# Kernel optimization log

Hardware: AMD Instinct MI355X
Metric: run time of the kernel (lower is better)

## Reference

```python
import jax, jax.numpy as jnp
import numpy as np

B, S, H, V, NL = 64, 2048, 512, 50257, 2

def setup_inputs() -> dict:
    key = jax.random.key(0)
    ks = jax.random.split(key, 20)
    s = 0.02
    return {
        "input_ids": jax.random.randint(ks[0], (B,), 0, V),
        "hidden": jax.random.normal(ks[1], (NL, B, H), jnp.float32),
        "block_attn_weights": jax.random.uniform(ks[2], (B, 32), jnp.float32),
        "encoder_outputs": jax.random.normal(ks[3], (B, S, H), jnp.float32),
        "n_blocks": 32,
        "emb": jax.random.normal(ks[4], (V, H), jnp.float32) * s,
        "attn_W": jax.random.normal(ks[5], (H, H), jnp.float32) * s,
        "attn_b": jnp.zeros((H,), jnp.float32),
        "W_ih0": jax.random.normal(ks[6], (3 * H, 2 * H), jnp.float32) * s,
        "W_hh0": jax.random.normal(ks[7], (3 * H, H), jnp.float32) * s,
        "b_ih0": jnp.zeros((3 * H,), jnp.float32),
        "b_hh0": jnp.zeros((3 * H,), jnp.float32),
        "W_ih1": jax.random.normal(ks[8], (3 * H, H), jnp.float32) * s,
        "W_hh1": jax.random.normal(ks[9], (3 * H, H), jnp.float32) * s,
        "b_ih1": jnp.zeros((3 * H,), jnp.float32),
        "b_hh1": jnp.zeros((3 * H,), jnp.float32),
        "out_W": jax.random.normal(ks[10], (V, 2 * H), jnp.float32) * s,
        "out_b": jnp.zeros((V,), jnp.float32),
    }

def _gru_cell(x, h, W_ih, W_hh, b_ih, b_hh):
    gx = x @ W_ih.T + b_ih            # [B, 3H]
    gh = h @ W_hh.T + b_hh            # [B, 3H]
    xr, xz, xn = jnp.split(gx, 3, axis=-1)
    hr, hz, hn = jnp.split(gh, 3, axis=-1)
    r = jax.nn.sigmoid(xr + hr)
    z = jax.nn.sigmoid(xz + hz)
    n = jnp.tanh(xn + r * hn)
    return (1.0 - z) * n + z * h

def reference(input_ids, hidden, block_attn_weights, encoder_outputs, n_blocks,
              emb, attn_W, attn_b, W_ih0, W_hh0, b_ih0, b_hh0,
              W_ih1, W_hh1, b_ih1, b_hh1, out_W, out_b):
    b, s, h = encoder_outputs.shape
    L = s // n_blocks
    eo = encoder_outputs.reshape(b, n_blocks, L, h)          # [B,N,L,H]
    # Luong general score: h_dec . (W e + b), per block
    energy = jnp.einsum('bnlh,gh->bnlg', eo, attn_W) + attn_b  # [B,N,L,H]
    scores = jnp.einsum('bh,bnlh->bnl', hidden[-1], energy)    # [B,N,L]
    attn_w = jax.nn.softmax(scores, axis=-1)                   # [B,N,L]
    block_ctx = jnp.einsum('bnl,bnlh->bnh', attn_w, eo)        # [B,N,H]
    context = jnp.einsum('bn,bnh->bh', block_attn_weights, block_ctx)  # [B,H]
    embedded = emb[input_ids]                                  # [B,H]
    x = jnp.concatenate([embedded, context], axis=-1)          # [B,2H]
    h0 = _gru_cell(x, hidden[0], W_ih0, W_hh0, b_ih0, b_hh0)
    h1 = _gru_cell(h0, hidden[1], W_ih1, W_hh1, b_ih1, b_hh1)
    new_hidden = jnp.stack([h0, h1], axis=0)                   # [NL,B,H]
    out_in = jnp.concatenate([h1, context], axis=-1)           # [B,2H]
    log_probs = jax.nn.log_softmax(out_in @ out_W.T + out_b, axis=-1)  # [B,V]
    return (log_probs, new_hidden, context, attn_w)
```

## Files before the change

### kernel.cpp

```cpp
#include <hip/hip_runtime.h>

#define B_  64
#define S_  2048
#define H_  512
#define V_  50257
#define NB_ 32
#define L_  64
#define H3_ 1536

typedef float  f32x4  __attribute__((ext_vector_type(4)));
typedef __bf16 bf16x8 __attribute__((ext_vector_type(8)));

struct alignas(16) U4 { unsigned int x, y, z, w; };

__device__ __forceinline__ unsigned int f2bf_bits(float f) {
  unsigned int u = __float_as_uint(f);
  return (u + 0x7fffu + ((u >> 16) & 1u)) >> 16;
}

__device__ __forceinline__ f32x4 ntload4(const float* p) {
  return __builtin_nontemporal_load((const f32x4*)p);
}

__device__ __forceinline__ float wave_sum(float v) {
#pragma unroll
  for (int off = 32; off > 0; off >>= 1) v += __shfl_xor(v, off, 64);
  return v;
}

__global__ __launch_bounds__(128) void k_q(const float* __restrict__ hidden,
                                           const float* __restrict__ attn_W,
                                           float* __restrict__ q) {
  __shared__ float sh[4 * H_];
  int tid = threadIdx.x;
  int h  = blockIdx.x * 128 + tid;
  int b0 = blockIdx.y * 4;
  const float* h1 = hidden + B_ * H_;
  for (int i = tid; i < 4 * H_; i += 128) sh[i] = h1[b0 * H_ + i];
  __syncthreads();
  float acc[4] = {0.f, 0.f, 0.f, 0.f};
  for (int g = 0; g < H_; ++g) {
    float w = attn_W[(size_t)g * H_ + h];
#pragma unroll
    for (int bb = 0; bb < 4; ++bb) acc[bb] += sh[bb * H_ + g] * w;
  }
#pragma unroll
  for (int bb = 0; bb < 4; ++bb) q[(b0 + bb) * H_ + h] = acc[bb];
}

__global__ __launch_bounds__(256) void k_attn(
    const float* __restrict__ eo, const float* __restrict__ hidden,
    const float* __restrict__ attn_b, const float* __restrict__ q,
    float* __restrict__ bc, float* __restrict__ attnw_out) {
  __shared__ float sm[4], ss[4];
  __shared__ float shA[4][H_];
  int tid = threadIdx.x;
  int wv = tid >> 6, lane = tid & 63;
  int idx = blockIdx.x;
  int b = idx >> 5, n = idx & 31;

  f32x4 q0 = *(const f32x4*)(q + (size_t)b * H_ + lane * 4);
  f32x4 q1 = *(const f32x4*)(q + (size_t)b * H_ + 256 + lane * 4);

  const float* hp = hidden + (size_t)B_ * H_ + (size_t)b * H_;
  f32x4 hx = *(const f32x4*)(hp + lane * 4);
  f32x4 hy = *(const f32x4*)(hp + 256 + lane * 4);
  f32x4 ax = *(const f32x4*)(attn_b + lane * 4);
  f32x4 ay = *(const f32x4*)(attn_b + 256 + lane * 4);
  float c0 = hx.x*ax.x + hx.y*ax.y + hx.z*ax.z + hx.w*ax.w
           + hy.x*ay.x + hy.y*ay.y + hy.z*ay.z + hy.w*ay.w;
  c0 = wave_sum(c0);

  const float* eb = eo + (size_t)(b * NB_ + n) * L_ * H_;
  float m = -1e30f, s = 0.f, myscore = 0.f;
  f32x4 A0 = {0,0,0,0}, A1 = {0,0,0,0};
  for (int lr = 0; lr < 16; lr += 2) {
    const float* rA = eb + (size_t)(wv * 16 + lr) * H_;
    const float* rB = rA + H_;
    f32x4 a0 = ntload4(rA + lane * 4);
    f32x4 a1 = ntload4(rA + 256 + lane * 4);
    f32x4 b0 = ntload4(rB + lane * 4);
    f32x4 b1 = ntload4(rB + 256 + lane * 4);
    float pa = a0.x*q0.x + a0.y*q0.y + a0.z*q0.z + a0.w*q0.w
             + a1.x*q1.x + a1.y*q1.y + a1.z*q1.z + a1.w*q1.w;
    float pb = b0.x*q0.x + b0.y*q0.y + b0.z*q0.z + b0.w*q0.w
             + b1.x*q1.x + b1.y*q1.y + b1.z*q1.z + b1.w*q1.w;
#pragma unroll
    for (int off = 32; off > 0; off >>= 1) {
      pa += __shfl_xor(pa, off, 64);
      pb += __shfl_xor(pb, off, 64);
    }
    pa += c0; pb += c0;
    if (lane == lr)     myscore = pa;
    if (lane == lr + 1) myscore = pb;
    float mnew  = fmaxf(m, fmaxf(pa, pb));
    float alpha = __expf(m - mnew);
    float wa    = __expf(pa - mnew);
    float wb    = __expf(pb - mnew);
    s = s * alpha + wa + wb;
    A0.x = A0.x*alpha + wa*a0.x + wb*b0.x;
    A0.y = A0.y*alpha + wa*a0.y + wb*b0.y;
    A0.z = A0.z*alpha + wa*a0.z + wb*b0.z;
    A0.w = A0.w*alpha + wa*a0.w + wb*b0.w;
    A1.x = A1.x*alpha + wa*a1.x + wb*b1.x;
    A1.y = A1.y*alpha + wa*a1.y + wb*b1.y;
    A1.z = A1.z*alpha + wa*a1.z + wb*b1.z;
    A1.w = A1.w*alpha + wa*a1.w + wb*b1.w;
    m = mnew;
  }
  if (lane == 0) { sm[wv] = m; ss[wv] = s; }
  __syncthreads();
  float m_g = fmaxf(fmaxf(sm[0], sm[1]), fmaxf(sm[2], sm[3]));
  float s_g = ss[0]*__expf(sm[0]-m_g) + ss[1]*__expf(sm[1]-m_g)
            + ss[2]*__expf(sm[2]-m_g) + ss[3]*__expf(sm[3]-m_g);
  float scale = __expf(m - m_g);
  f32x4* pa4 = (f32x4*)&shA[wv][0];
  f32x4 w0 = {A0.x*scale, A0.y*scale, A0.z*scale, A0.w*scale};
  f32x4 w1 = {A1.x*scale, A1.y*scale, A1.z*scale, A1.w*scale};
  pa4[lane] = w0; pa4[64 + lane] = w1;
  __syncthreads();
  float inv = 1.f / s_g;
  float2 sum = {0.f, 0.f};
#pragma unroll
  for (int w = 0; w < 4; ++w) {
    float2 v = ((float2*)&shA[w][0])[tid];
    sum.x += v.x; sum.y += v.y;
  }
  float2* bv = (float2*)(bc + (size_t)(b * NB_ + n) * H_);
  bv[tid] = (float2){sum.x * inv, sum.y * inv};
  if (lane < 16)
    attnw_out[(size_t)(b * NB_ + n) * L_ + wv * 16 + lane] =
        __expf(myscore - m_g) * inv;
}

__global__ __launch_bounds__(512) void k_prep(
    const int* __restrict__ ids, const float* __restrict__ hidden,
    const float* __restrict__ baw, const float* __restrict__ emb,
    const float* __restrict__ bc, float* __restrict__ ctx,
    unsigned short* __restrict__ xcatb, unsigned short* __restrict__ h0b,
    unsigned short* __restrict__ h1b, float* __restrict__ out_ctx) {
  int b = blockIdx.x, h = threadIdx.x;
  int id = ids[b];
  float ev = emb[(size_t)id * H_ + h];
  float acc = 0.f;
  for (int n = 0; n < NB_; ++n)
    acc += baw[b * NB_ + n] * bc[(size_t)(b * NB_ + n) * H_ + h];
  ctx[b * H_ + h]      = acc;
  out_ctx[b * H_ + h]  = acc;
  xcatb[b * 1024 + h]        = (unsigned short)f2bf_bits(ev);
  xcatb[b * 1024 + 512 + h]  = (unsigned short)f2bf_bits(acc);
  h0b[b * H_ + h] = (unsigned short)f2bf_bits(hidden[b * H_ + h]);
  h1b[b * H_ + h] = (unsigned short)f2bf_bits(hidden[B_ * H_ + b * H_ + h]);
}

__global__ __launch_bounds__(256) void k_mv2(
    const float* __restrict__ W1, const float* __restrict__ bias1,
    const unsigned short* __restrict__ A1, float* __restrict__ C1, int K1,
    const float* __restrict__ W2, const float* __restrict__ bias2,
    const unsigned short* __restrict__ A2, float* __restrict__ C2, int K2) {
  bool sec = blockIdx.x >= 96;
  const float* W = sec ? W2 : W1;
  const float* bias = sec ? bias2 : bias1;
  const unsigned short* A = sec ? A2 : A1;
  float* C = sec ? C2 : C1;
  int K = sec ? K2 : K1;
  int blk = sec ? blockIdx.x - 96 : blockIdx.x;

  int tid = threadIdx.x;
  int wv = tid >> 6, lane = tid & 63;
  int mrow = lane & 15, qd = lane >> 4;
  int j = blk * 16 + mrow;
  const unsigned short* ap = A + (size_t)(wv * 16 + mrow) * K + qd * 8;
  const float* wp = W + (size_t)j * K + qd * 8;
  f32x4 acc = (f32x4){0.f, 0.f, 0.f, 0.f};
  for (int k0 = 0; k0 < K; k0 += 32) {
    bf16x8 af = __builtin_bit_cast(bf16x8, *(const U4*)(ap + k0));
    f32x4 w0 = *(const f32x4*)(wp + k0);
    f32x4 w1 = *(const f32x4*)(wp + k0 + 4);
    U4 braw;
    braw.x = f2bf_bits(w0.x) | (f2bf_bits(w0.y) << 16);
    braw.y = f2bf_bits(w0.z) | (f2bf_bits(w0.w) << 16);
    braw.z = f2bf_bits(w1.x) | (f2bf_bits(w1.y) << 16);
    braw.w = f2bf_bits(w1.z) | (f2bf_bits(w1.w) << 16);
    bf16x8 bf = __builtin_bit_cast(bf16x8, braw);
    acc = __builtin_amdgcn_mfma_f32_16x16x32_bf16(af, bf, acc, 0, 0, 0);
  }
  float bv = bias[j];
#pragma unroll
  for (int r = 0; r < 4; ++r) {
    int brow = wv * 16 + qd * 4 + r;
    C[(size_t)brow * H3_ + j] = acc[r] + bv;
  }
}

__global__ __launch_bounds__(256) void k_out(
    const float* __restrict__ W, const float* __restrict__ bias,
    const unsigned short* __restrict__ A, float* __restrict__ C) {
  int tid = threadIdx.x;
  int wv = tid >> 6, lane = tid & 63;
  int mrow = lane & 15, qd = lane >> 4;
  int j = blockIdx.x * 64 + wv * 16 + mrow;
  int jc = j < V_ ? j : V_ - 1;
  const float* wp = W + (size_t)jc * 1024 + qd * 8;
  const unsigned short* ap = A + mrow * 1024 + qd * 8;
  f32x4 acc[4];
#pragma unroll
  for (int r = 0; r < 4; ++r) acc[r] = (f32x4){0.f, 0.f, 0.f, 0.f};
  for (int k0 = 0; k0 < 1024; k0 += 32) {
    f32x4 w0 = ntload4(wp + k0);
    f32x4 w1 = ntload4(wp + k0 + 4);
    U4 braw;
    braw.x = f2bf_bits(w0.x) | (f2bf_bits(w0.y) << 16);
    braw.y = f2bf_bits(w0.z) | (f2bf_bits(w0.w) << 16);
    braw.z = f2bf_bits(w1.x) | (f2bf_bits(w1.y) << 16);
    braw.w = f2bf_bits(w1.z) | (f2bf_bits(w1.w) << 16);
    bf16x8 bw = __builtin_bit_cast(bf16x8, braw);
#pragma unroll
    for (int r = 0; r < 4; ++r) {
      bf16x8 af = __builtin_bit_cast(bf16x8, *(const U4*)(ap + r * 16 * 1024 + k0));
      acc[r] = __builtin_amdgcn_mfma_f32_16x16x32_bf16(af, bw, acc[r], 0, 0, 0);
    }
  }
  if (j < V_) {
    float bv = bias[j];
#pragma unroll
    for (int r = 0; r < 4; ++r) {
#pragma unroll
      for (int g = 0; g < 4; ++g) {
        int brow = r * 16 + qd * 4 + g;
        C[(size_t)brow * V_ + j] = acc[r][g] + bv;
      }
    }
  }
}

__global__ __launch_bounds__(512) void k_gru(
    const float* __restrict__ gx, const float* __restrict__ gh,
    const float* __restrict__ hprev, float* __restrict__ hnew_out,
    unsigned short* __restrict__ hnew_bf, const float* __restrict__ ctx,
    unsigned short* __restrict__ outin) {
  int b = blockIdx.x, i = threadIdx.x;
  size_t g0 = (size_t)b * H3_ + i;
  float xr = gx[g0], xz = gx[g0 + 512], xn = gx[g0 + 1024];
  float hr = gh[g0], hz = gh[g0 + 512], hn = gh[g0 + 1024];
  float r  = 1.f / (1.f + __expf(-(xr + hr)));
  float z  = 1.f / (1.f + __expf(-(xz + hz)));
  float nn = tanhf(xn + r * hn);
  float hp = hprev[b * H_ + i];
  float h  = (1.f - z) * nn + z * hp;
  hnew_out[b * H_ + i] = h;
  hnew_bf[b * H_ + i]  = (unsigned short)f2bf_bits(h);
  if (outin) {
    outin[b * 1024 + i]       = (unsigned short)f2bf_bits(h);
    outin[b * 1024 + 512 + i] = (unsigned short)f2bf_bits(ctx[b * H_ + i]);
  }
}

__global__ __launch_bounds__(1024) void k_lsm(const float* __restrict__ logits,
                                              float* __restrict__ out) {
  int b = blockIdx.x, tid = threadIdx.x;
  int lane = tid & 63, wid = tid >> 6;
  const float* row = logits + (size_t)b * V_;
  __shared__ float redm[16], reds[16], bl[1];
  float m_t = -1e30f, s_t = 0.f;
  for (int j = tid; j < V_; j += 1024) {
    float x = row[j];
    if (x > m_t) {
      s_t = s_t * __expf(m_t - x) + 1.f;
      m_t = x;
    } else {
      s_t += __expf(x - m_t);
    }
  }
#pragma unroll
  for (int off = 32; off > 0; off >>= 1) {
    float mo = __shfl_xor(m_t, off, 64);
    float so = __shfl_xor(s_t, off, 64);
    float mn = fmaxf(m_t, mo);
    s_t = s_t * __expf(m_t - mn) + so * __expf(mo - mn);
    m_t = mn;
  }
  if (lane == 0) { redm[wid] = m_t; reds[wid] = s_t; }
  __syncthreads();
  if (tid == 0) {
    float m_g = redm[0], s_g = reds[0];
    for (int i = 1; i < 16; ++i) {
      float mn = fmaxf(m_g, redm[i]);
      s_g = s_g * __expf(m_g - mn) + reds[i] * __expf(redm[i] - mn);
      m_g = mn;
    }
    bl[0] = m_g + logf(s_g);
  }
  __syncthreads();
  float lse = bl[0];
  float* orow = out + (size_t)b * V_;
  for (int j = tid; j < V_; j += 1024)
    __builtin_nontemporal_store(row[j] - lse, orow + j);
}

extern "C" void kernel_launch(void* const* d_in, const int* in_sizes, int n_in,
                              void* d_out, int out_size, void* d_ws, size_t ws_size,
                              hipStream_t stream) {
  const int*   ids    = (const int*)d_in[0];
  const float* hidden = (const float*)d_in[1];
  const float* baw    = (const float*)d_in[2];
  const float* eo     = (const float*)d_in[3];
  const float* emb    = (const float*)d_in[5];
  const float* attn_W = (const float*)d_in[6];
  const float* attn_b = (const float*)d_in[7];
  const float* W_ih0  = (const float*)d_in[8];
  const float* W_hh0  = (const float*)d_in[9];
  const float* b_ih0  = (const float*)d_in[10];
  const float* b_hh0  = (const float*)d_in[11];
  const float* W_ih1  = (const float*)d_in[12];
  const float* W_hh1  = (const float*)d_in[13];
  const float* b_ih1  = (const float*)d_in[14];
  const float* b_hh1  = (const float*)d_in[15];
  const float* out_W  = (const float*)d_in[16];
  const float* out_b  = (const float*)d_in[17];
  float* out = (float*)d_out;

  char* ws = (char*)d_ws;
  float*          q      = (float*)(ws + 0);
  float*          bc     = (float*)(ws + 131072);
  float*          ctx    = (float*)(ws + 4325376);
  unsigned short* xcatb  = (unsigned short*)(ws + 4456448);
  unsigned short* h0b    = (unsigned short*)(ws + 4587520);
  unsigned short* h1b    = (unsigned short*)(ws + 4653056);
  unsigned short* h0nb   = (unsigned short*)(ws + 4718592);
  unsigned short* outinb = (unsigned short*)(ws + 4784128);
  float*          gx     = (float*)(ws + 4915200);
  float*          gh     = (float*)(ws + 5308416);
  float*          logits = (float*)(ws + 5701632);

  float* out_lp   = out;
  float* out_nh   = out + 3216448;
  float* out_ctx  = out + 3281984;
  float* out_attw = out + 3314752;

  k_q   <<<dim3(4, 16), 128, 0, stream>>>(hidden, attn_W, q);
  k_attn<<<2048, 256, 0, stream>>>(eo, hidden, attn_b, q, bc, out_attw);
  k_prep<<<64, 512, 0, stream>>>(ids, hidden, baw, emb, bc, ctx, xcatb, h0b, h1b, out_ctx);

  k_mv2<<<192, 256, 0, stream>>>(W_ih0, b_ih0, xcatb, gx, 1024,
                                 W_hh0, b_hh0, h0b,   gh, 512);
  k_gru<<<64, 512, 0, stream>>>(gx, gh, hidden, out_nh, h0nb,
                                (const float*)nullptr, (unsigned short*)nullptr);

  k_mv2<<<192, 256, 0, stream>>>(W_ih1, b_ih1, h0nb, gx, 512,
                                 W_hh1, b_hh1, h1b,  gh, 512);
  k_gru<<<64, 512, 0, stream>>>(gx, gh, hidden + B_ * H_, out_nh + B_ * H_, h0nb,
                                ctx, outinb);

  k_out<<<786, 256, 0, stream>>>(out_W, out_b, outinb, logits);
  k_lsm<<<64, 1024, 0, stream>>>(logits, out_lp);
}
```

Before: 690.7 us.

## Fuse per-block softmax stats into output GEMM and widen attention blocks

The output projection kernel now computes per-block row max and sum-exp partials and writes them to workspace. A small kernel combines these into a per-row log-sum-exp, and a wide elementwise kernel then writes logits minus lse. This replaces the 64-block log-softmax that read the logits twice with low parallelism. Separately, the attention kernel moves to 512 threads with 8 waves, each handling 8 rows instead of 16, to raise parallelism per block. The cost is an extra launch plus a shared-memory reduction and syncthreads at the end of the output GEMM.

```diff
diff --git a/kernel.cpp b/kernel.cpp
--- a/kernel.cpp
+++ b/kernel.cpp
@@ -7,6 +7,7 @@
 #define NB_ 32
 #define L_  64
 #define H3_ 1536
+#define NBLK_OUT 786
 
 typedef float  f32x4  __attribute__((ext_vector_type(4)));
 typedef __bf16 bf16x8 __attribute__((ext_vector_type(8)));
@@ -48,12 +49,12 @@
   for (int bb = 0; bb < 4; ++bb) q[(b0 + bb) * H_ + h] = acc[bb];
 }
 
-__global__ __launch_bounds__(256) void k_attn(
+__global__ __launch_bounds__(512) void k_attn(
     const float* __restrict__ eo, const float* __restrict__ hidden,
     const float* __restrict__ attn_b, const float* __restrict__ q,
     float* __restrict__ bc, float* __restrict__ attnw_out) {
-  __shared__ float sm[4], ss[4];
-  __shared__ float shA[4][H_];
+  __shared__ float sm[8], ss[8];
+  __shared__ float shA[8][H_];
   int tid = threadIdx.x;
   int wv = tid >> 6, lane = tid & 63;
   int idx = blockIdx.x;
@@ -74,8 +75,8 @@
   const float* eb = eo + (size_t)(b * NB_ + n) * L_ * H_;
   float m = -1e30f, s = 0.f, myscore = 0.f;
   f32x4 A0 = {0,0,0,0}, A1 = {0,0,0,0};
-  for (int lr = 0; lr < 16; lr += 2) {
-    const float* rA = eb + (size_t)(wv * 16 + lr) * H_;
+  for (int lr = 0; lr < 8; lr += 2) {
+    const float* rA = eb + (size_t)(wv * 8 + lr) * H_;
     const float* rB = rA + H_;
     f32x4 a0 = ntload4(rA + lane * 4);
     f32x4 a1 = ntload4(rA + 256 + lane * 4);
@@ -110,9 +111,12 @@
   }
   if (lane == 0) { sm[wv] = m; ss[wv] = s; }
   __syncthreads();
-  float m_g = fmaxf(fmaxf(sm[0], sm[1]), fmaxf(sm[2], sm[3]));
-  float s_g = ss[0]*__expf(sm[0]-m_g) + ss[1]*__expf(sm[1]-m_g)
-            + ss[2]*__expf(sm[2]-m_g) + ss[3]*__expf(sm[3]-m_g);
+  float m_g = sm[0];
+#pragma unroll
+  for (int w = 1; w < 8; ++w) m_g = fmaxf(m_g, sm[w]);
+  float s_g = 0.f;
+#pragma unroll
+  for (int w = 0; w < 8; ++w) s_g += ss[w] * __expf(sm[w] - m_g);
   float scale = __expf(m - m_g);
   f32x4* pa4 = (f32x4*)&shA[wv][0];
   f32x4 w0 = {A0.x*scale, A0.y*scale, A0.z*scale, A0.w*scale};
@@ -120,16 +124,12 @@
   pa4[lane] = w0; pa4[64 + lane] = w1;
   __syncthreads();
   float inv = 1.f / s_g;
-  float2 sum = {0.f, 0.f};
-#pragma unroll
-  for (int w = 0; w < 4; ++w) {
-    float2 v = ((float2*)&shA[w][0])[tid];
-    sum.x += v.x; sum.y += v.y;
-  }
-  float2* bv = (float2*)(bc + (size_t)(b * NB_ + n) * H_);
-  bv[tid] = (float2){sum.x * inv, sum.y * inv};
-  if (lane < 16)
-    attnw_out[(size_t)(b * NB_ + n) * L_ + wv * 16 + lane] =
+  float sum = 0.f;
+#pragma unroll
+  for (int w = 0; w < 8; ++w) sum += shA[w][tid];
+  bc[(size_t)(b * NB_ + n) * H_ + tid] = sum * inv;
+  if (lane < 8)
+    attnw_out[(size_t)(b * NB_ + n) * L_ + wv * 8 + lane] =
         __expf(myscore - m_g) * inv;
 }
 
@@ -195,7 +195,9 @@
 
 __global__ __launch_bounds__(256) void k_out(
     const float* __restrict__ W, const float* __restrict__ bias,
-    const unsigned short* __restrict__ A, float* __restrict__ C) {
+    const unsigned short* __restrict__ A, float* __restrict__ C,
+    float* __restrict__ pm, float* __restrict__ ps) {
+  __shared__ float lmS[4][64], lsS[4][64];
   int tid = threadIdx.x;
   int wv = tid >> 6, lane = tid & 63;
   int mrow = lane & 15, qd = lane >> 4;
@@ -221,8 +223,8 @@
       acc[r] = __builtin_amdgcn_mfma_f32_16x16x32_bf16(af, bw, acc[r], 0, 0, 0);
     }
   }
+  float bv = (j < V_) ? bias[j] : 0.f;
   if (j < V_) {
-    float bv = bias[j];
 #pragma unroll
     for (int r = 0; r < 4; ++r) {
 #pragma unroll
@@ -231,6 +233,39 @@
         C[(size_t)brow * V_ + j] = acc[r][g] + bv;
       }
     }
+  }
+#pragma unroll
+  for (int r = 0; r < 4; ++r) {
+#pragma unroll
+    for (int g = 0; g < 4; ++g) {
+      float v = (j < V_) ? acc[r][g] + bv : -1e30f;
+      float mm = v;
+#pragma unroll
+      for (int off = 1; off <= 8; off <<= 1)
+        mm = fmaxf(mm, __shfl_xor(mm, off, 64));
+      float se = __expf(v - mm);
+#pragma unroll
+      for (int off = 1; off <= 8; off <<= 1)
+        se += __shfl_xor(se, off, 64);
+      if (mrow == 0) {
+        int brow = r * 16 + qd * 4 + g;
+        lmS[wv][brow] = mm;
+        lsS[wv][brow] = se;
+      }
+    }
+  }
+  __syncthreads();
+  if (tid < 64) {
+    float m = lmS[0][tid], s = lsS[0][tid];
+#pragma unroll
+    for (int w = 1; w < 4; ++w) {
+      float mk = lmS[w][tid], sk = lsS[w][tid];
+      float mn = fmaxf(m, mk);
+      s = s * __expf(m - mn) + sk * __expf(mk - mn);
+      m = mn;
+    }
+    pm[(size_t)tid * NBLK_OUT + blockIdx.x] = m;
+    ps[(size_t)tid * NBLK_OUT + blockIdx.x] = s;
   }
 }
 
@@ -256,46 +291,49 @@
   }
 }
 
-__global__ __launch_bounds__(1024) void k_lsm(const float* __restrict__ logits,
-                                              float* __restrict__ out) {
-  int b = blockIdx.x, tid = threadIdx.x;
-  int lane = tid & 63, wid = tid >> 6;
-  const float* row = logits + (size_t)b * V_;
-  __shared__ float redm[16], reds[16], bl[1];
-  float m_t = -1e30f, s_t = 0.f;
-  for (int j = tid; j < V_; j += 1024) {
-    float x = row[j];
-    if (x > m_t) {
-      s_t = s_t * __expf(m_t - x) + 1.f;
-      m_t = x;
-    } else {
-      s_t += __expf(x - m_t);
-    }
+__global__ __launch_bounds__(256) void k_lse(const float* __restrict__ pm,
+                                             const float* __restrict__ ps,
+                                             float* __restrict__ lse) {
+  __shared__ float rm[4], rs[4];
+  int b = blockIdx.x, tid = threadIdx.x, lane = tid & 63, wid = tid >> 6;
+  float m = -1e30f, s = 0.f;
+  for (int k = tid; k < NBLK_OUT; k += 256) {
+    float mk = pm[(size_t)b * NBLK_OUT + k];
+    float sk = ps[(size_t)b * NBLK_OUT + k];
+    float mn = fmaxf(m, mk);
+    s = s * __expf(m - mn) + sk * __expf(mk - mn);
+    m = mn;
   }
 #pragma unroll
   for (int off = 32; off > 0; off >>= 1) {
-    float mo = __shfl_xor(m_t, off, 64);
-    float so = __shfl_xor(s_t, off, 64);
-    float mn = fmaxf(m_t, mo);
-    s_t = s_t * __expf(m_t - mn) + so * __expf(mo - mn);
-    m_t = mn;
-  }
-  if (lane == 0) { redm[wid] = m_t; reds[wid] = s_t; }
+    float mo = __shfl_xor(m, off, 64);
+    float so = __shfl_xor(s, off, 64);
+    float mn = fmaxf(m, mo);
+    s = s * __expf(m - mn) + so * __expf(mo - mn);
+    m = mn;
+  }
+  if (lane == 0) { rm[wid] = m; rs[wid] = s; }
   __syncthreads();
   if (tid == 0) {
-    float m_g = redm[0], s_g = reds[0];
-    for (int i = 1; i < 16; ++i) {
-      float mn = fmaxf(m_g, redm[i]);
-      s_g = s_g * __expf(m_g - mn) + reds[i] * __expf(redm[i] - mn);
-      m_g = mn;
-    }
-    bl[0] = m_g + logf(s_g);
-  }
-  __syncthreads();
-  float lse = bl[0];
-  float* orow = out + (size_t)b * V_;
-  for (int j = tid; j < V_; j += 1024)
-    __builtin_nontemporal_store(row[j] - lse, orow + j);
+    float mg = rm[0], sg = rs[0];
+    for (int w = 1; w < 4; ++w) {
+      float mn = fmaxf(mg, rm[w]);
+      sg = sg * __expf(mg - mn) + rs[w] * __expf(rm[w] - mn);
+      mg = mn;
+    }
+    lse[b] = mg + logf(sg);
+  }
+}
+
+__global__ __launch_bounds__(256) void k_wlp(const float* __restrict__ logits,
+                                             const float* __restrict__ lse,
+                                             float* __restrict__ out) {
+  int b = blockIdx.y;
+  int j = blockIdx.x * 256 + threadIdx.x;
+  if (j < V_) {
+    float v = __builtin_nontemporal_load(logits + (size_t)b * V_ + j);
+    __builtin_nontemporal_store(v - lse[b], out + (size_t)b * V_ + j);
+  }
 }
 
 extern "C" void kernel_launch(void* const* d_in, const int* in_sizes, int n_in,
@@ -332,6 +370,9 @@
   float*          gx     = (float*)(ws + 4915200);
   float*          gh     = (float*)(ws + 5308416);
   float*          logits = (float*)(ws + 5701632);
+  float*          pm     = (float*)(ws + 18567424);
+  float*          ps     = (float*)(ws + 18768640);
+  float*          lse    = (float*)(ws + 18969856);
 
   float* out_lp   = out;
   float* out_nh   = out + 3216448;
@@ -339,7 +380,7 @@
   float* out_attw = out + 3314752;
 
   k_q   <<<dim3(4, 16), 128, 0, stream>>>(hidden, attn_W, q);
-  k_attn<<<2048, 256, 0, stream>>>(eo, hidden, attn_b, q, bc, out_attw);
+  k_attn<<<2048, 512, 0, stream>>>(eo, hidden, attn_b, q, bc, out_attw);
   k_prep<<<64, 512, 0, stream>>>(ids, hidden, baw, emb, bc, ctx, xcatb, h0b, h1b, out_ctx);
 
   k_mv2<<<192, 256, 0, stream>>>(W_ih0, b_ih0, xcatb, gx, 1024,
@@ -352,6 +393,7 @@
   k_gru<<<64, 512, 0, stream>>>(gx, gh, hidden + B_ * H_, out_nh + B_ * H_, h0nb,
                                 ctx, outinb);
 
-  k_out<<<786, 256, 0, stream>>>(out_W, out_b, outinb, logits);
-  k_lsm<<<64, 1024, 0, stream>>>(logits, out_lp);
-}
+  k_out<<<NBLK_OUT, 256, 0, stream>>>(out_W, out_b, outinb, logits, pm, ps);
+  k_lse<<<64, 256, 0, stream>>>(pm, ps, lse);
+  k_wlp<<<dim3(197, 64), 256, 0, stream>>>(logits, lse, out_lp);
+}
```

Measured after the change: 678.6 us. Within noise of the previous version (-1.8%).
